# Performance work log

Measured on AMD Instinct MI355X. Metric: run time of the kernel, lower is better.

## Reference

```python
import jax, jax.numpy as jnp
import numpy as np

K_ORDER = 3
GRID_N = 10
GRID_LO, GRID_HI = -2.0, 2.0
LAYERS = [(49, 256), (256, 256), (256, 10)]
NCOEF = GRID_N + K_ORDER  # 13


def mish(x):
    return x * jnp.tanh(jax.nn.softplus(x))


def bspline_basis(x):
    # x: (B, in) -> basis (B, in, GRID_N + K_ORDER)
    h = (GRID_HI - GRID_LO) / GRID_N
    knots = GRID_LO + h * jnp.arange(-K_ORDER, GRID_N + K_ORDER + 1, dtype=x.dtype)  # (G+2k+1,)
    xx = x[..., None]
    B = ((xx >= knots[:-1]) & (xx < knots[1:])).astype(x.dtype)  # degree-0, (B,in,G+2k)
    for d in range(1, K_ORDER + 1):
        left = (xx - knots[: -(d + 1)]) / (knots[d:-1] - knots[: -(d + 1)]) * B[..., :-1]
        right = (knots[d + 1:] - xx) / (knots[d + 1:] - knots[1:-d]) * B[..., 1:]
        B = left + right
    return B  # (B, in, G+k)


def kan_layer(x, coef, scale_base, scale_sp, bias):
    # x: (B,in); coef: (in,out,G+k); scales: (in,out); bias: (out,)
    basis = bspline_basis(x)                                   # (B,in,G+k)
    spline = jnp.einsum('big,iog->bo', basis, coef * scale_sp[..., None])
    base = jnp.einsum('bi,io->bo', mish(x), scale_base)
    return base + spline + bias


def setup_inputs() -> dict:
    key = jax.random.key(0)
    ks = jax.random.split(key, 1 + 4 * len(LAYERS))
    inp = {'x': jax.random.normal(ks[0], (8192, 1, 28, 28), dtype=jnp.float32)}
    i = 1
    for li, (fin, fout) in enumerate(LAYERS, start=1):
        inp[f'coef{li}'] = 0.1 * jax.random.normal(ks[i], (fin, fout, NCOEF), dtype=jnp.float32); i += 1
        inp[f'sb{li}'] = 1.0 + 0.1 * jax.random.normal(ks[i], (fin, fout), dtype=jnp.float32); i += 1
        inp[f'sp{li}'] = 1.0 + 0.1 * jax.random.normal(ks[i], (fin, fout), dtype=jnp.float32); i += 1
        inp[f'b{li}'] = jnp.zeros((fout,), dtype=jnp.float32); i += 1
    return inp


def reference(x, coef1, sb1, sp1, b1, coef2, sb2, sp2, b2, coef3, sb3, sp3, b3):
    B = x.shape[0]
    # avg_pool2d(x, 4): 28x28 -> 7x7
    h = x.reshape(B, 1, 7, 4, 7, 4).mean(axis=(3, 5))
    h = h.reshape(B, 49)
    h = kan_layer(h, coef1, sb1, sp1, b1)
    h = kan_layer(h, coef2, sb2, sp2, b2)
    h = kan_layer(h, coef3, sb3, sp3, b3)
    return jax.nn.log_softmax(h, axis=1)
```

## Files before the change

### kernel.cpp

```cpp
#include <hip/hip_runtime.h>
#include <hip/hip_bf16.h>

typedef __bf16 bf16x8_t __attribute__((ext_vector_type(8)));
typedef float f32x4_t __attribute__((ext_vector_type(4)));
using bf16 = __hip_bfloat16;

__device__ __forceinline__ unsigned short f2bf_bits(float v) {
  __hip_bfloat16 h = __float2bfloat16(v);
  return *reinterpret_cast<unsigned short*>(&h);
}

__device__ __forceinline__ float mish_f(float x) {
  float z = __expf(x);
  float n = z * (z + 2.0f);
  float m = x * n / (n + 2.0f);
  return (x > 10.0f) ? x : m;
}

__device__ __forceinline__ void kan_feats28(bf16* dst, float x) {
  unsigned int* d32 = (unsigned int*)dst;
#pragma unroll
  for (int d = 0; d < 7; ++d) d32[d] = 0u;
  float t = (x + 3.2f) * 2.5f;
  if (t >= 0.0f && t < 16.0f) {
    float tf = floorf(t);
    int c = (int)tf;
    float u = t - tf;
    float um = 1.0f - u;
    float u2 = u * u, u3 = u2 * u;
    const float s6 = 1.0f / 6.0f;
    float w0 = um * um * um * s6;
    float w1 = (3.0f * u3 - 6.0f * u2 + 4.0f) * s6;
    float w2 = (-3.0f * u3 + 3.0f * u2 + 3.0f * u + 1.0f) * s6;
    float w3 = u3 * s6;
    int j0 = c - 3;
    if (j0 >= 0)               dst[j0]     = __float2bfloat16(w0);
    if (j0 >= -1 && j0 <= 11)  dst[j0 + 1] = __float2bfloat16(w1);
    if (j0 >= -2 && j0 <= 10)  dst[j0 + 2] = __float2bfloat16(w2);
    if (j0 <= 9)               dst[j0 + 3] = __float2bfloat16(w3);
  }
  dst[13] = __float2bfloat16(mish_f(x));
}

__global__ __launch_bounds__(256) void prep_all(
    const float* __restrict__ c1, const float* __restrict__ sb1, const float* __restrict__ sp1,
    const float* __restrict__ c2, const float* __restrict__ sb2, const float* __restrict__ sp2,
    const float* __restrict__ c3, const float* __restrict__ sb3, const float* __restrict__ sp3,
    bf16* __restrict__ W1f, bf16* __restrict__ W2f, bf16* __restrict__ W3f) {
  const int b = blockIdx.x, t = threadIdx.x;
  float vals[14];
  if (b < 49) {
    const int i = b, o = t;
    const int ntg = o >> 4, lrr = o & 15;
    const size_t io = (size_t)i * 256 + o;
    const float spv = sp1[io];
#pragma unroll
    for (int r = 0; r < 13; ++r) vals[r] = c1[io * 13 + r] * spv;
    vals[13] = sb1[io];
#pragma unroll
    for (int d = 0; d < 7; ++d) {
      const int k2 = i * 14 + 2 * d;
      const int s = k2 >> 5, r2 = k2 & 31;
      const size_t off = ((size_t)(s * 16 + ntg)) * 512 + lrr * 32 + (r2 >> 3) * 8 + (r2 & 7);
      *(unsigned int*)(W1f + off) = (unsigned int)f2bf_bits(vals[2 * d]) |
                                    ((unsigned int)f2bf_bits(vals[2 * d + 1]) << 16);
    }
  } else if (b == 49) {
    const int ntg = t >> 4, lrr = t & 15;
#pragma unroll
    for (int d = 0; d < 9; ++d) {
      const int k2 = 686 + 2 * d;
      const int r2 = k2 & 31;
      *(unsigned int*)(W1f + ((size_t)(21 * 16 + ntg)) * 512 + lrr * 32 + (r2 >> 3) * 8 + (r2 & 7)) = 0u;
    }
  } else if (b < 562) {
    if (t >= 128) return;
    const int idx = b - 50;
    const int i = idx >> 1;
    const int o = (idx & 1) * 128 + t;
    const int ntg = o >> 4, lrr = o & 15;
    const size_t io = (size_t)i * 256 + o;
    const float spv = sp2[io];
#pragma unroll
    for (int r = 0; r < 13; ++r) vals[r] = c2[io * 13 + r] * spv;
    vals[13] = sb2[io];
#pragma unroll
    for (int d = 0; d < 7; ++d) {
      const int k2 = i * 14 + 2 * d;
      const int s = k2 >> 5, r2 = k2 & 31;
      const size_t off = ((size_t)(s * 16 + ntg)) * 512 + lrr * 32 + (r2 >> 3) * 8 + (r2 & 7);
      *(unsigned int*)(W2f + off) = (unsigned int)f2bf_bits(vals[2 * d]) |
                                    ((unsigned int)f2bf_bits(vals[2 * d + 1]) << 16);
    }
  } else {
    const int i = b - 562, o = t;
    if (o < 10) {
      const size_t io = (size_t)i * 10 + o;
      const float spv = sp3[io];
#pragma unroll
      for (int r = 0; r < 13; ++r) vals[r] = c3[io * 13 + r] * spv;
      vals[13] = sb3[io];
#pragma unroll
      for (int d = 0; d < 7; ++d) {
        const int k2 = i * 14 + 2 * d;
        const int s = k2 >> 5, r2 = k2 & 31;
        const size_t off = (size_t)s * 512 + o * 32 + (r2 >> 3) * 8 + (r2 & 7);
        *(unsigned int*)(W3f + off) = (unsigned int)f2bf_bits(vals[2 * d]) |
                                      ((unsigned int)f2bf_bits(vals[2 * d + 1]) << 16);
      }
    } else if (o < 16) {
#pragma unroll
      for (int d = 0; d < 7; ++d) {
        const int k2 = i * 14 + 2 * d;
        const int s = k2 >> 5, r2 = k2 & 31;
        *(unsigned int*)(W3f + (size_t)s * 512 + o * 32 + (r2 >> 3) * 8 + (r2 & 7)) = 0u;
      }
    }
  }
}

__global__ __launch_bounds__(1024, 4) void meganet(
    const float* __restrict__ x, const bf16* __restrict__ W1f,
    const bf16* __restrict__ W2f, const bf16* __restrict__ W3f,
    const float* __restrict__ b1, const float* __restrict__ b2,
    const float* __restrict__ b3, float* __restrict__ out) {
  __shared__ __align__(16) char lds[73728];
  float* const Hs = (float*)lds;
  bf16* const Ach0 = (bf16*)(lds + 36864);
  bf16* const Ach1 = (bf16*)(lds + 51712);
  float* const P = (float*)(lds + 66560);
  float* const xs = (float*)lds;
  float* const Red = (float*)(lds + 36864);
  float* const V = (float*)(lds + 51712);

  const int t = threadIdx.x;
  const int w = t >> 6, lane = t & 63, quad = lane >> 4, lr = lane & 15;
  const int tr = (t >> 4) & 31, ej = t & 15;
  const int r0 = blockIdx.x * 32;
  const int foff = lr * 32 + quad * 8;
  const bool cons = (w < 8);
  const int ntg0 = 2 * w;

  for (int h = 0; h < 2; ++h) {
    const float4* src = (const float4*)x + (size_t)(r0 + h * 16) * 196;
    float4* xd = (float4*)xs;
#pragma unroll
    for (int l = 0; l < 4; ++l) {
      const int idx = t + l * 1024;
      if (idx < 3136) xd[idx] = src[idx];
    }
    __syncthreads();
    if (t < 784) {
      const int img = t / 49, p = t - img * 49;
      const int oh = p / 7, ow = p - oh * 7;
      const float* xi = xs + img * 784 + oh * 112 + ow * 4;
      float s = 0.f;
#pragma unroll
      for (int rr = 0; rr < 4; ++rr)
#pragma unroll
        for (int cc = 0; cc < 4; ++cc) s += xi[rr * 28 + cc];
      P[(h * 16 + img) * 56 + p] = s * (1.0f / 16.0f);
    }
    __syncthreads();
  }

  f32x4_t acc[2][2];
#pragma unroll
  for (int m = 0; m < 2; ++m)
#pragma unroll
    for (int n = 0; n < 2; ++n) acc[m][n] = (f32x4_t){0.f, 0.f, 0.f, 0.f};

  bf16x8_t q0[4], q1[4];
  if (cons) {
#pragma unroll
    for (int s = 0; s < 4; ++s) {
      q0[s] = *(const bf16x8_t*)(W1f + (size_t)(s * 16 + ntg0) * 512 + foff);
      q1[s] = *(const bf16x8_t*)(W1f + (size_t)(s * 16 + ntg0 + 1) * 512 + foff);
    }
  } else {
    kan_feats28(Ach0 + tr * 232 + ej * 14, P[tr * 56 + ej]);
  }
  __syncthreads();
#pragma unroll
  for (int c = 0; c < 4; ++c) {
    const bf16* const Ac = (c & 1) ? Ach1 : Ach0;
    bf16* const An = (c & 1) ? Ach0 : Ach1;
    if (cons) {
      const int nks = (c < 3) ? 7 : 1;
#pragma unroll
      for (int ks = 0; ks < 7; ++ks) {
        if (ks >= nks) continue;
        const int kk = c * 7 + ks;
        const int sl = kk & 3;
        bf16x8_t bb0 = q0[sl], bb1 = q1[sl];
        if (kk + 4 < 22) {
          q0[sl] = *(const bf16x8_t*)(W1f + (size_t)((kk + 4) * 16 + ntg0) * 512 + foff);
          q1[sl] = *(const bf16x8_t*)(W1f + (size_t)((kk + 4) * 16 + ntg0 + 1) * 512 + foff);
        }
#pragma unroll
        for (int m = 0; m < 2; ++m) {
          bf16x8_t a = *(const bf16x8_t*)(Ac + (m * 16 + lr) * 232 + ks * 32 + quad * 8);
          acc[m][0] = __builtin_amdgcn_mfma_f32_16x16x32_bf16(a, bb0, acc[m][0], 0, 0, 0);
          acc[m][1] = __builtin_amdgcn_mfma_f32_16x16x32_bf16(a, bb1, acc[m][1], 0, 0, 0);
        }
      }
    } else {
      if (c < 2) {
        kan_feats28(An + tr * 232 + ej * 14, P[tr * 56 + (c + 1) * 16 + ej]);
      } else if (c == 2) {
        if (ej == 0) kan_feats28(An + tr * 232, P[tr * 56 + 48]);
        else if (ej == 1) {
          unsigned int* z = (unsigned int*)(An + tr * 232 + 14);
#pragma unroll
          for (int d = 0; d < 9; ++d) z[d] = 0u;
        }
      }
    }
    __syncthreads();
  }
  if (cons) {
#pragma unroll
    for (int m = 0; m < 2; ++m)
#pragma unroll
      for (int n = 0; n < 2; ++n) {
        const int col = w * 32 + n * 16 + lr;
        const float bn = b1[col];
        f32x4_t v;
#pragma unroll
        for (int r = 0; r < 4; ++r) v[r] = acc[m][n][r] + bn;
        *(f32x4_t*)(Hs + col * 36 + m * 16 + quad * 4) = v;
      }
  }
  __syncthreads();

#pragma unroll
  for (int m = 0; m < 2; ++m)
#pragma unroll
    for (int n = 0; n < 2; ++n) acc[m][n] = (f32x4_t){0.f, 0.f, 0.f, 0.f};
  if (cons) {
#pragma unroll
    for (int s = 0; s < 4; ++s) {
      q0[s] = *(const bf16x8_t*)(W2f + (size_t)(s * 16 + ntg0) * 512 + foff);
      q1[s] = *(const bf16x8_t*)(W2f + (size_t)(s * 16 + ntg0 + 1) * 512 + foff);
    }
  } else {
    kan_feats28(Ach0 + tr * 232 + ej * 14, Hs[ej * 36 + tr]);
  }
  __syncthreads();
#pragma unroll
  for (int c = 0; c < 16; ++c) {
    const bf16* const Ac = (c & 1) ? Ach1 : Ach0;
    bf16* const An = (c & 1) ? Ach0 : Ach1;
    if (cons) {
#pragma unroll
      for (int ks = 0; ks < 7; ++ks) {
        const int kk = c * 7 + ks;
        const int sl = kk & 3;
        bf16x8_t bb0 = q0[sl], bb1 = q1[sl];
        if (kk + 4 < 112) {
          q0[sl] = *(const bf16x8_t*)(W2f + (size_t)((kk + 4) * 16 + ntg0) * 512 + foff);
          q1[sl] = *(const bf16x8_t*)(W2f + (size_t)((kk + 4) * 16 + ntg0 + 1) * 512 + foff);
        }
#pragma unroll
        for (int m = 0; m < 2; ++m) {
          bf16x8_t a = *(const bf16x8_t*)(Ac + (m * 16 + lr) * 232 + ks * 32 + quad * 8);
          acc[m][0] = __builtin_amdgcn_mfma_f32_16x16x32_bf16(a, bb0, acc[m][0], 0, 0, 0);
          acc[m][1] = __builtin_amdgcn_mfma_f32_16x16x32_bf16(a, bb1, acc[m][1], 0, 0, 0);
        }
      }
    } else if (c < 15) {
      kan_feats28(An + tr * 232 + ej * 14, Hs[((c + 1) * 16 + ej) * 36 + tr]);
    }
    __syncthreads();
  }
  if (cons) {
#pragma unroll
    for (int m = 0; m < 2; ++m)
#pragma unroll
      for (int n = 0; n < 2; ++n) {
        const int col = w * 32 + n * 16 + lr;
        const float bn = b2[col];
        f32x4_t v;
#pragma unroll
        for (int r = 0; r < 4; ++r) v[r] = acc[m][n][r] + bn;
        *(f32x4_t*)(Hs + col * 36 + m * 16 + quad * 4) = v;
      }
  }
  __syncthreads();

  f32x4_t acc3[2];
  acc3[0] = (f32x4_t){0.f, 0.f, 0.f, 0.f};
  acc3[1] = acc3[0];
  bf16x8_t q3[4];
  if (w < 7) {
#pragma unroll
    for (int s = 0; s < 4; ++s)
      q3[s] = *(const bf16x8_t*)(W3f + (size_t)(s * 7 + w) * 512 + foff);
  } else if (!cons) {
    kan_feats28(Ach0 + tr * 232 + ej * 14, Hs[ej * 36 + tr]);
  }
  __syncthreads();
#pragma unroll
  for (int c = 0; c < 16; ++c) {
    const bf16* const Ac = (c & 1) ? Ach1 : Ach0;
    bf16* const An = (c & 1) ? Ach0 : Ach1;
    if (w < 7) {
      bf16x8_t bb = q3[c & 3];
      if (c + 4 < 16)
        q3[c & 3] = *(const bf16x8_t*)(W3f + (size_t)((c + 4) * 7 + w) * 512 + foff);
#pragma unroll
      for (int m = 0; m < 2; ++m) {
        bf16x8_t a = *(const bf16x8_t*)(Ac + (m * 16 + lr) * 232 + w * 32 + quad * 8);
        acc3[m] = __builtin_amdgcn_mfma_f32_16x16x32_bf16(a, bb, acc3[m], 0, 0, 0);
      }
    } else if (!cons && c < 15) {
      kan_feats28(An + tr * 232 + ej * 14, Hs[((c + 1) * 16 + ej) * 36 + tr]);
    }
    __syncthreads();
  }
  if (w < 7) {
#pragma unroll
    for (int m = 0; m < 2; ++m)
#pragma unroll
      for (int r = 0; r < 4; ++r)
        Red[w * 512 + (m * 16 + quad * 4 + r) * 16 + lr] = acc3[m][r];
  }
  __syncthreads();
  if (t < 512) {
    float s = (ej < 10) ? b3[ej] : 0.f;
#pragma unroll
    for (int ks = 0; ks < 7; ++ks) s += Red[ks * 512 + tr * 16 + ej];
    V[tr * 16 + ej] = s;
  }
  __syncthreads();
  if (t < 32) {
    float vv[10];
#pragma unroll
    for (int o = 0; o < 10; ++o) vv[o] = V[t * 16 + o];
    float mx = vv[0];
#pragma unroll
    for (int o = 1; o < 10; ++o) mx = fmaxf(mx, vv[o]);
    float se = 0.f;
#pragma unroll
    for (int o = 0; o < 10; ++o) se += expf(vv[o] - mx);
    const float l = mx + logf(se);
#pragma unroll
    for (int o = 0; o < 10; ++o) out[(size_t)(r0 + t) * 10 + o] = vv[o] - l;
  }
}

extern "C" void kernel_launch(void* const* d_in, const int* in_sizes, int n_in,
                              void* d_out, int out_size, void* d_ws, size_t ws_size,
                              hipStream_t stream) {
  const float* x = (const float*)d_in[0];
  const float* coef1 = (const float*)d_in[1];
  const float* sb1 = (const float*)d_in[2];
  const float* sp1 = (const float*)d_in[3];
  const float* b1 = (const float*)d_in[4];
  const float* coef2 = (const float*)d_in[5];
  const float* sb2 = (const float*)d_in[6];
  const float* sp2 = (const float*)d_in[7];
  const float* b2 = (const float*)d_in[8];
  const float* coef3 = (const float*)d_in[9];
  const float* sb3 = (const float*)d_in[10];
  const float* sp3 = (const float*)d_in[11];
  const float* b3 = (const float*)d_in[12];
  float* out = (float*)d_out;

  char* ws = (char*)d_ws;
  bf16* W1f = (bf16*)ws;
  bf16* W2f = (bf16*)(ws + 360448);
  bf16* W3f = (bf16*)(ws + 2195456);

  prep_all<<<818, 256, 0, stream>>>(coef1, sb1, sp1, coef2, sb2, sp2,
                                    coef3, sb3, sp3, W1f, W2f, W3f);
  meganet<<<256, 1024, 0, stream>>>(x, W1f, W2f, W3f, b1, b2, b3, out);
}
```

Baseline: 139.0 us.

## Double chunk size in layers 2-3, halve barriers, use lightweight LDS-only barrier

Layers 2 and 3 now process 32 input features per chunk instead of 16, so the producer waves build two feature rows each step and the number of block barriers in those loops is halved. The LDS A-tile stride grows to 474 and shared memory grows to about 102 KB to hold the larger double buffers. The weight prefetch depth in layer 2 rises from 4 to 6 slots. __syncthreads is replaced by a custom barrier that waits only on lgkmcnt, not on outstanding global loads. The larger LDS footprint may reduce blocks per CU, and the custom barrier depends on no global-memory ordering being needed across it.

```diff
diff --git a/kernel.cpp b/kernel.cpp
--- a/kernel.cpp
+++ b/kernel.cpp
@@ -4,6 +4,10 @@
 typedef __bf16 bf16x8_t __attribute__((ext_vector_type(8)));
 typedef float f32x4_t __attribute__((ext_vector_type(4)));
 using bf16 = __hip_bfloat16;
+
+__device__ __forceinline__ void softbar() {
+  asm volatile("s_waitcnt lgkmcnt(0)\n\ts_barrier" ::: "memory");
+}
 
 __device__ __forceinline__ unsigned short f2bf_bits(float v) {
   __hip_bfloat16 h = __float2bfloat16(v);
@@ -124,14 +128,14 @@
     const bf16* __restrict__ W2f, const bf16* __restrict__ W3f,
     const float* __restrict__ b1, const float* __restrict__ b2,
     const float* __restrict__ b3, float* __restrict__ out) {
-  __shared__ __align__(16) char lds[73728];
+  __shared__ __align__(16) char lds[104704];
   float* const Hs = (float*)lds;
   bf16* const Ach0 = (bf16*)(lds + 36864);
-  bf16* const Ach1 = (bf16*)(lds + 51712);
-  float* const P = (float*)(lds + 66560);
+  bf16* const Ach1 = (bf16*)(lds + 67200);
+  float* const P = (float*)(lds + 97536);
   float* const xs = (float*)lds;
   float* const Red = (float*)(lds + 36864);
-  float* const V = (float*)(lds + 51712);
+  float* const V = (float*)(lds + 51200);
 
   const int t = threadIdx.x;
   const int w = t >> 6, lane = t & 63, quad = lane >> 4, lr = lane & 15;
@@ -149,7 +153,7 @@
       const int idx = t + l * 1024;
       if (idx < 3136) xd[idx] = src[idx];
     }
-    __syncthreads();
+    softbar();
     if (t < 784) {
       const int img = t / 49, p = t - img * 49;
       const int oh = p / 7, ow = p - oh * 7;
@@ -161,7 +165,7 @@
         for (int cc = 0; cc < 4; ++cc) s += xi[rr * 28 + cc];
       P[(h * 16 + img) * 56 + p] = s * (1.0f / 16.0f);
     }
-    __syncthreads();
+    softbar();
   }
 
   f32x4_t acc[2][2];
@@ -170,7 +174,8 @@
 #pragma unroll
     for (int n = 0; n < 2; ++n) acc[m][n] = (f32x4_t){0.f, 0.f, 0.f, 0.f};
 
-  bf16x8_t q0[4], q1[4];
+  bf16x8_t q0[6], q1[6];
+
   if (cons) {
 #pragma unroll
     for (int s = 0; s < 4; ++s) {
@@ -178,9 +183,9 @@
       q1[s] = *(const bf16x8_t*)(W1f + (size_t)(s * 16 + ntg0 + 1) * 512 + foff);
     }
   } else {
-    kan_feats28(Ach0 + tr * 232 + ej * 14, P[tr * 56 + ej]);
-  }
-  __syncthreads();
+    kan_feats28(Ach0 + tr * 474 + ej * 14, P[tr * 56 + ej]);
+  }
+  softbar();
 #pragma unroll
   for (int c = 0; c < 4; ++c) {
     const bf16* const Ac = (c & 1) ? Ach1 : Ach0;
@@ -199,24 +204,24 @@
         }
 #pragma unroll
         for (int m = 0; m < 2; ++m) {
-          bf16x8_t a = *(const bf16x8_t*)(Ac + (m * 16 + lr) * 232 + ks * 32 + quad * 8);
+          bf16x8_t a = *(const bf16x8_t*)(Ac + (m * 16 + lr) * 474 + ks * 32 + quad * 8);
           acc[m][0] = __builtin_amdgcn_mfma_f32_16x16x32_bf16(a, bb0, acc[m][0], 0, 0, 0);
           acc[m][1] = __builtin_amdgcn_mfma_f32_16x16x32_bf16(a, bb1, acc[m][1], 0, 0, 0);
         }
       }
     } else {
       if (c < 2) {
-        kan_feats28(An + tr * 232 + ej * 14, P[tr * 56 + (c + 1) * 16 + ej]);
+        kan_feats28(An + tr * 474 + ej * 14, P[tr * 56 + (c + 1) * 16 + ej]);
       } else if (c == 2) {
-        if (ej == 0) kan_feats28(An + tr * 232, P[tr * 56 + 48]);
+        if (ej == 0) kan_feats28(An + tr * 474, P[tr * 56 + 48]);
         else if (ej == 1) {
-          unsigned int* z = (unsigned int*)(An + tr * 232 + 14);
+          unsigned int* z = (unsigned int*)(An + tr * 474 + 14);
 #pragma unroll
           for (int d = 0; d < 9; ++d) z[d] = 0u;
         }
       }
     }
-    __syncthreads();
+    softbar();
   }
   if (cons) {
 #pragma unroll
@@ -231,7 +236,7 @@
         *(f32x4_t*)(Hs + col * 36 + m * 16 + quad * 4) = v;
       }
   }
-  __syncthreads();
+  softbar();
 
 #pragma unroll
   for (int m = 0; m < 2; ++m)
@@ -239,39 +244,42 @@
     for (int n = 0; n < 2; ++n) acc[m][n] = (f32x4_t){0.f, 0.f, 0.f, 0.f};
   if (cons) {
 #pragma unroll
-    for (int s = 0; s < 4; ++s) {
+    for (int s = 0; s < 6; ++s) {
       q0[s] = *(const bf16x8_t*)(W2f + (size_t)(s * 16 + ntg0) * 512 + foff);
       q1[s] = *(const bf16x8_t*)(W2f + (size_t)(s * 16 + ntg0 + 1) * 512 + foff);
     }
   } else {
-    kan_feats28(Ach0 + tr * 232 + ej * 14, Hs[ej * 36 + tr]);
-  }
-  __syncthreads();
-#pragma unroll
-  for (int c = 0; c < 16; ++c) {
+    kan_feats28(Ach0 + tr * 474 + ej * 14, Hs[ej * 36 + tr]);
+    kan_feats28(Ach0 + tr * 474 + (ej + 16) * 14, Hs[(ej + 16) * 36 + tr]);
+  }
+  softbar();
+#pragma unroll
+  for (int c = 0; c < 8; ++c) {
     const bf16* const Ac = (c & 1) ? Ach1 : Ach0;
     bf16* const An = (c & 1) ? Ach0 : Ach1;
     if (cons) {
 #pragma unroll
-      for (int ks = 0; ks < 7; ++ks) {
-        const int kk = c * 7 + ks;
-        const int sl = kk & 3;
+      for (int j = 0; j < 14; ++j) {
+        const int kk = c * 14 + j;
+        const int sl = kk % 6;
         bf16x8_t bb0 = q0[sl], bb1 = q1[sl];
-        if (kk + 4 < 112) {
-          q0[sl] = *(const bf16x8_t*)(W2f + (size_t)((kk + 4) * 16 + ntg0) * 512 + foff);
-          q1[sl] = *(const bf16x8_t*)(W2f + (size_t)((kk + 4) * 16 + ntg0 + 1) * 512 + foff);
+        if (kk + 6 < 112) {
+          q0[sl] = *(const bf16x8_t*)(W2f + (size_t)((kk + 6) * 16 + ntg0) * 512 + foff);
+          q1[sl] = *(const bf16x8_t*)(W2f + (size_t)((kk + 6) * 16 + ntg0 + 1) * 512 + foff);
         }
 #pragma unroll
         for (int m = 0; m < 2; ++m) {
-          bf16x8_t a = *(const bf16x8_t*)(Ac + (m * 16 + lr) * 232 + ks * 32 + quad * 8);
+          bf16x8_t a = *(const bf16x8_t*)(Ac + (m * 16 + lr) * 474 + j * 32 + quad * 8);
           acc[m][0] = __builtin_amdgcn_mfma_f32_16x16x32_bf16(a, bb0, acc[m][0], 0, 0, 0);
           acc[m][1] = __builtin_amdgcn_mfma_f32_16x16x32_bf16(a, bb1, acc[m][1], 0, 0, 0);
         }
       }
-    } else if (c < 15) {
-      kan_feats28(An + tr * 232 + ej * 14, Hs[((c + 1) * 16 + ej) * 36 + tr]);
-    }
-    __syncthreads();
+    } else if (c < 7) {
+      const int i0 = (c + 1) * 32 + ej;
+      kan_feats28(An + tr * 474 + ej * 14, Hs[i0 * 36 + tr]);
+      kan_feats28(An + tr * 474 + (ej + 16) * 14, Hs[(i0 + 16) * 36 + tr]);
+    }
+    softbar();
   }
   if (cons) {
 #pragma unroll
@@ -286,7 +294,7 @@
         *(f32x4_t*)(Hs + col * 36 + m * 16 + quad * 4) = v;
       }
   }
-  __syncthreads();
+  softbar();
 
   f32x4_t acc3[2];
   acc3[0] = (f32x4_t){0.f, 0.f, 0.f, 0.f};
@@ -294,29 +302,39 @@
   bf16x8_t q3[4];
   if (w < 7) {
 #pragma unroll
-    for (int s = 0; s < 4; ++s)
-      q3[s] = *(const bf16x8_t*)(W3f + (size_t)(s * 7 + w) * 512 + foff);
+    for (int cc = 0; cc < 2; ++cc) {
+      q3[cc * 2] = *(const bf16x8_t*)(W3f + (size_t)(cc * 14 + w) * 512 + foff);
+      q3[cc * 2 + 1] = *(const bf16x8_t*)(W3f + (size_t)(cc * 14 + 7 + w) * 512 + foff);
+    }
   } else if (!cons) {
-    kan_feats28(Ach0 + tr * 232 + ej * 14, Hs[ej * 36 + tr]);
-  }
-  __syncthreads();
-#pragma unroll
-  for (int c = 0; c < 16; ++c) {
+    kan_feats28(Ach0 + tr * 474 + ej * 14, Hs[ej * 36 + tr]);
+    kan_feats28(Ach0 + tr * 474 + (ej + 16) * 14, Hs[(ej + 16) * 36 + tr]);
+  }
+  softbar();
+#pragma unroll
+  for (int c = 0; c < 8; ++c) {
     const bf16* const Ac = (c & 1) ? Ach1 : Ach0;
     bf16* const An = (c & 1) ? Ach0 : Ach1;
     if (w < 7) {
-      bf16x8_t bb = q3[c & 3];
-      if (c + 4 < 16)
-        q3[c & 3] = *(const bf16x8_t*)(W3f + (size_t)((c + 4) * 7 + w) * 512 + foff);
+      const int p = (c & 1) * 2;
+      bf16x8_t bb0 = q3[p], bb1 = q3[p + 1];
+      if (c + 2 < 8) {
+        q3[p] = *(const bf16x8_t*)(W3f + (size_t)((c + 2) * 14 + w) * 512 + foff);
+        q3[p + 1] = *(const bf16x8_t*)(W3f + (size_t)((c + 2) * 14 + 7 + w) * 512 + foff);
+      }
 #pragma unroll
       for (int m = 0; m < 2; ++m) {
-        bf16x8_t a = *(const bf16x8_t*)(Ac + (m * 16 + lr) * 232 + w * 32 + quad * 8);
-        acc3[m] = __builtin_amdgcn_mfma_f32_16x16x32_bf16(a, bb, acc3[m], 0, 0, 0);
-      }
-    } else if (!cons && c < 15) {
-      kan_feats28(An + tr * 232 + ej * 14, Hs[((c + 1) * 16 + ej) * 36 + tr]);
-    }
-    __syncthreads();
+        bf16x8_t a0 = *(const bf16x8_t*)(Ac + (m * 16 + lr) * 474 + w * 32 + quad * 8);
+        bf16x8_t a1 = *(const bf16x8_t*)(Ac + (m * 16 + lr) * 474 + (7 + w) * 32 + quad * 8);
+        acc3[m] = __builtin_amdgcn_mfma_f32_16x16x32_bf16(a0, bb0, acc3[m], 0, 0, 0);
+        acc3[m] = __builtin_amdgcn_mfma_f32_16x16x32_bf16(a1, bb1, acc3[m], 0, 0, 0);
+      }
+    } else if (!cons && c < 7) {
+      const int i0 = (c + 1) * 32 + ej;
+      kan_feats28(An + tr * 474 + ej * 14, Hs[i0 * 36 + tr]);
+      kan_feats28(An + tr * 474 + (ej + 16) * 14, Hs[(i0 + 16) * 36 + tr]);
+    }
+    softbar();
   }
   if (w < 7) {
 #pragma unroll
@@ -325,14 +343,14 @@
       for (int r = 0; r < 4; ++r)
         Red[w * 512 + (m * 16 + quad * 4 + r) * 16 + lr] = acc3[m][r];
   }
-  __syncthreads();
+  softbar();
   if (t < 512) {
     float s = (ej < 10) ? b3[ej] : 0.f;
 #pragma unroll
     for (int ks = 0; ks < 7; ++ks) s += Red[ks * 512 + tr * 16 + ej];
     V[tr * 16 + ej] = s;
   }
-  __syncthreads();
+  softbar();
   if (t < 32) {
     float vv[10];
 #pragma unroll
```

Measured after the change: 185.2 us. +33.3%, slower.

## Halve rows per block and merge producer/consumer warps in fused KAN kernel

Applied to the files above, without the earlier changes.

The fused KAN kernel now handles 16 rows per block with 512 threads instead of 32 rows with 1024 threads, and launches 512 blocks instead of 256. The separate producer warps that built B-spline features are removed. All 8 warps now run the MFMAs, and the first 256 threads also compute the next chunk's features after their MFMAs. This halves LDS use and doubles the grid to spread work over more CUs. In exchange, each weight fetch from global memory/L2 is reused over half as many rows, and feature building is no longer overlapped by dedicated warps.

```diff
diff --git a/kernel.cpp b/kernel.cpp
--- a/kernel.cpp
+++ b/kernel.cpp
@@ -119,38 +119,37 @@
   }
 }
 
-__global__ __launch_bounds__(1024, 4) void meganet(
+__global__ __launch_bounds__(512, 4) void meganet(
     const float* __restrict__ x, const bf16* __restrict__ W1f,
     const bf16* __restrict__ W2f, const bf16* __restrict__ W3f,
     const float* __restrict__ b1, const float* __restrict__ b2,
     const float* __restrict__ b3, float* __restrict__ out) {
-  __shared__ __align__(16) char lds[73728];
+  __shared__ __align__(16) char lds[38912];
   float* const Hs = (float*)lds;
-  bf16* const Ach0 = (bf16*)(lds + 36864);
-  bf16* const Ach1 = (bf16*)(lds + 51712);
-  float* const P = (float*)(lds + 66560);
+  bf16* const Ach0 = (bf16*)(lds + 20480);
+  bf16* const Ach1 = (bf16*)(lds + 27904);
+  float* const P = (float*)(lds + 35328);
   float* const xs = (float*)lds;
-  float* const Red = (float*)(lds + 36864);
-  float* const V = (float*)(lds + 51712);
+  float* const Red = (float*)(lds + 20480);
+  float* const V = (float*)(lds + 27904);
 
   const int t = threadIdx.x;
   const int w = t >> 6, lane = t & 63, quad = lane >> 4, lr = lane & 15;
-  const int tr = (t >> 4) & 31, ej = t & 15;
-  const int r0 = blockIdx.x * 32;
+  const int tr = (t >> 4) & 15, ej = t & 15;
+  const int r0 = blockIdx.x * 16;
   const int foff = lr * 32 + quad * 8;
-  const bool cons = (w < 8);
   const int ntg0 = 2 * w;
 
   for (int h = 0; h < 2; ++h) {
-    const float4* src = (const float4*)x + (size_t)(r0 + h * 16) * 196;
+    const float4* src = (const float4*)x + (size_t)(r0 + h * 8) * 196;
     float4* xd = (float4*)xs;
 #pragma unroll
     for (int l = 0; l < 4; ++l) {
-      const int idx = t + l * 1024;
-      if (idx < 3136) xd[idx] = src[idx];
-    }
-    __syncthreads();
-    if (t < 784) {
+      const int idx = t + l * 512;
+      if (idx < 1568) xd[idx] = src[idx];
+    }
+    __syncthreads();
+    if (t < 392) {
       const int img = t / 49, p = t - img * 49;
       const int oh = p / 7, ow = p - oh * 7;
       const float* xi = xs + img * 784 + oh * 112 + ow * 4;
@@ -159,52 +158,43 @@
       for (int rr = 0; rr < 4; ++rr)
 #pragma unroll
         for (int cc = 0; cc < 4; ++cc) s += xi[rr * 28 + cc];
-      P[(h * 16 + img) * 56 + p] = s * (1.0f / 16.0f);
-    }
-    __syncthreads();
-  }
-
-  f32x4_t acc[2][2];
-#pragma unroll
-  for (int m = 0; m < 2; ++m)
-#pragma unroll
-    for (int n = 0; n < 2; ++n) acc[m][n] = (f32x4_t){0.f, 0.f, 0.f, 0.f};
-
+      P[(h * 8 + img) * 56 + p] = s * (1.0f / 16.0f);
+    }
+    __syncthreads();
+  }
+
+  f32x4_t acc[2];
+  acc[0] = (f32x4_t){0.f, 0.f, 0.f, 0.f};
+  acc[1] = acc[0];
   bf16x8_t q0[4], q1[4];
-  if (cons) {
-#pragma unroll
-    for (int s = 0; s < 4; ++s) {
-      q0[s] = *(const bf16x8_t*)(W1f + (size_t)(s * 16 + ntg0) * 512 + foff);
-      q1[s] = *(const bf16x8_t*)(W1f + (size_t)(s * 16 + ntg0 + 1) * 512 + foff);
-    }
-  } else {
-    kan_feats28(Ach0 + tr * 232 + ej * 14, P[tr * 56 + ej]);
-  }
+
+#pragma unroll
+  for (int s = 0; s < 4; ++s) {
+    q0[s] = *(const bf16x8_t*)(W1f + (size_t)(s * 16 + ntg0) * 512 + foff);
+    q1[s] = *(const bf16x8_t*)(W1f + (size_t)(s * 16 + ntg0 + 1) * 512 + foff);
+  }
+  if (t < 256) kan_feats28(Ach0 + tr * 232 + ej * 14, P[tr * 56 + ej]);
   __syncthreads();
 #pragma unroll
   for (int c = 0; c < 4; ++c) {
     const bf16* const Ac = (c & 1) ? Ach1 : Ach0;
     bf16* const An = (c & 1) ? Ach0 : Ach1;
-    if (cons) {
-      const int nks = (c < 3) ? 7 : 1;
-#pragma unroll
-      for (int ks = 0; ks < 7; ++ks) {
-        if (ks >= nks) continue;
-        const int kk = c * 7 + ks;
-        const int sl = kk & 3;
-        bf16x8_t bb0 = q0[sl], bb1 = q1[sl];
-        if (kk + 4 < 22) {
-          q0[sl] = *(const bf16x8_t*)(W1f + (size_t)((kk + 4) * 16 + ntg0) * 512 + foff);
-          q1[sl] = *(const bf16x8_t*)(W1f + (size_t)((kk + 4) * 16 + ntg0 + 1) * 512 + foff);
-        }
-#pragma unroll
-        for (int m = 0; m < 2; ++m) {
-          bf16x8_t a = *(const bf16x8_t*)(Ac + (m * 16 + lr) * 232 + ks * 32 + quad * 8);
-          acc[m][0] = __builtin_amdgcn_mfma_f32_16x16x32_bf16(a, bb0, acc[m][0], 0, 0, 0);
-          acc[m][1] = __builtin_amdgcn_mfma_f32_16x16x32_bf16(a, bb1, acc[m][1], 0, 0, 0);
-        }
-      }
-    } else {
+    const int nks = (c < 3) ? 7 : 1;
+#pragma unroll
+    for (int ks = 0; ks < 7; ++ks) {
+      if (ks >= nks) continue;
+      const int kk = c * 7 + ks;
+      const int sl = kk & 3;
+      bf16x8_t bb0 = q0[sl], bb1 = q1[sl];
+      if (kk + 4 < 22) {
+        q0[sl] = *(const bf16x8_t*)(W1f + (size_t)((kk + 4) * 16 + ntg0) * 512 + foff);
+        q1[sl] = *(const bf16x8_t*)(W1f + (size_t)((kk + 4) * 16 + ntg0 + 1) * 512 + foff);
+      }
+      bf16x8_t a = *(const bf16x8_t*)(Ac + lr * 232 + ks * 32 + quad * 8);
+      acc[0] = __builtin_amdgcn_mfma_f32_16x16x32_bf16(a, bb0, acc[0], 0, 0, 0);
+      acc[1] = __builtin_amdgcn_mfma_f32_16x16x32_bf16(a, bb1, acc[1], 0, 0, 0);
+    }
+    if (t < 256) {
       if (c < 2) {
         kan_feats28(An + tr * 232 + ej * 14, P[tr * 56 + (c + 1) * 16 + ej]);
       } else if (c == 2) {
@@ -218,87 +208,66 @@
     }
     __syncthreads();
   }
-  if (cons) {
-#pragma unroll
-    for (int m = 0; m < 2; ++m)
-#pragma unroll
-      for (int n = 0; n < 2; ++n) {
-        const int col = w * 32 + n * 16 + lr;
-        const float bn = b1[col];
-        f32x4_t v;
-#pragma unroll
-        for (int r = 0; r < 4; ++r) v[r] = acc[m][n][r] + bn;
-        *(f32x4_t*)(Hs + col * 36 + m * 16 + quad * 4) = v;
-      }
-  }
-  __syncthreads();
-
-#pragma unroll
-  for (int m = 0; m < 2; ++m)
-#pragma unroll
-    for (int n = 0; n < 2; ++n) acc[m][n] = (f32x4_t){0.f, 0.f, 0.f, 0.f};
-  if (cons) {
-#pragma unroll
-    for (int s = 0; s < 4; ++s) {
-      q0[s] = *(const bf16x8_t*)(W2f + (size_t)(s * 16 + ntg0) * 512 + foff);
-      q1[s] = *(const bf16x8_t*)(W2f + (size_t)(s * 16 + ntg0 + 1) * 512 + foff);
-    }
-  } else {
-    kan_feats28(Ach0 + tr * 232 + ej * 14, Hs[ej * 36 + tr]);
-  }
+#pragma unroll
+  for (int n = 0; n < 2; ++n) {
+    const int col = w * 32 + n * 16 + lr;
+    const float bn = b1[col];
+    f32x4_t v;
+#pragma unroll
+    for (int r = 0; r < 4; ++r) v[r] = acc[n][r] + bn;
+    *(f32x4_t*)(Hs + col * 20 + quad * 4) = v;
+  }
+  __syncthreads();
+
+  acc[0] = (f32x4_t){0.f, 0.f, 0.f, 0.f};
+  acc[1] = acc[0];
+#pragma unroll
+  for (int s = 0; s < 4; ++s) {
+    q0[s] = *(const bf16x8_t*)(W2f + (size_t)(s * 16 + ntg0) * 512 + foff);
+    q1[s] = *(const bf16x8_t*)(W2f + (size_t)(s * 16 + ntg0 + 1) * 512 + foff);
+  }
+  if (t < 256) kan_feats28(Ach0 + tr * 232 + ej * 14, Hs[ej * 20 + tr]);
   __syncthreads();
 #pragma unroll
   for (int c = 0; c < 16; ++c) {
     const bf16* const Ac = (c & 1) ? Ach1 : Ach0;
     bf16* const An = (c & 1) ? Ach0 : Ach1;
-    if (cons) {
-#pragma unroll
-      for (int ks = 0; ks < 7; ++ks) {
-        const int kk = c * 7 + ks;
-        const int sl = kk & 3;
-        bf16x8_t bb0 = q0[sl], bb1 = q1[sl];
-        if (kk + 4 < 112) {
-          q0[sl] = *(const bf16x8_t*)(W2f + (size_t)((kk + 4) * 16 + ntg0) * 512 + foff);
-          q1[sl] = *(const bf16x8_t*)(W2f + (size_t)((kk + 4) * 16 + ntg0 + 1) * 512 + foff);
-        }
-#pragma unroll
-        for (int m = 0; m < 2; ++m) {
-          bf16x8_t a = *(const bf16x8_t*)(Ac + (m * 16 + lr) * 232 + ks * 32 + quad * 8);
-          acc[m][0] = __builtin_amdgcn_mfma_f32_16x16x32_bf16(a, bb0, acc[m][0], 0, 0, 0);
-          acc[m][1] = __builtin_amdgcn_mfma_f32_16x16x32_bf16(a, bb1, acc[m][1], 0, 0, 0);
-        }
-      }
-    } else if (c < 15) {
-      kan_feats28(An + tr * 232 + ej * 14, Hs[((c + 1) * 16 + ej) * 36 + tr]);
-    }
-    __syncthreads();
-  }
-  if (cons) {
-#pragma unroll
-    for (int m = 0; m < 2; ++m)
-#pragma unroll
-      for (int n = 0; n < 2; ++n) {
-        const int col = w * 32 + n * 16 + lr;
-        const float bn = b2[col];
-        f32x4_t v;
-#pragma unroll
-        for (int r = 0; r < 4; ++r) v[r] = acc[m][n][r] + bn;
-        *(f32x4_t*)(Hs + col * 36 + m * 16 + quad * 4) = v;
-      }
-  }
-  __syncthreads();
-
-  f32x4_t acc3[2];
-  acc3[0] = (f32x4_t){0.f, 0.f, 0.f, 0.f};
-  acc3[1] = acc3[0];
+#pragma unroll
+    for (int ks = 0; ks < 7; ++ks) {
+      const int kk = c * 7 + ks;
+      const int sl = kk & 3;
+      bf16x8_t bb0 = q0[sl], bb1 = q1[sl];
+      if (kk + 4 < 112) {
+        q0[sl] = *(const bf16x8_t*)(W2f + (size_t)((kk + 4) * 16 + ntg0) * 512 + foff);
+        q1[sl] = *(const bf16x8_t*)(W2f + (size_t)((kk + 4) * 16 + ntg0 + 1) * 512 + foff);
+      }
+      bf16x8_t a = *(const bf16x8_t*)(Ac + lr * 232 + ks * 32 + quad * 8);
+      acc[0] = __builtin_amdgcn_mfma_f32_16x16x32_bf16(a, bb0, acc[0], 0, 0, 0);
+      acc[1] = __builtin_amdgcn_mfma_f32_16x16x32_bf16(a, bb1, acc[1], 0, 0, 0);
+    }
+    if (t < 256 && c < 15)
+      kan_feats28(An + tr * 232 + ej * 14, Hs[((c + 1) * 16 + ej) * 20 + tr]);
+    __syncthreads();
+  }
+#pragma unroll
+  for (int n = 0; n < 2; ++n) {
+    const int col = w * 32 + n * 16 + lr;
+    const float bn = b2[col];
+    f32x4_t v;
+#pragma unroll
+    for (int r = 0; r < 4; ++r) v[r] = acc[n][r] + bn;
+    *(f32x4_t*)(Hs + col * 20 + quad * 4) = v;
+  }
+  __syncthreads();
+
+  f32x4_t acc3 = {0.f, 0.f, 0.f, 0.f};
   bf16x8_t q3[4];
   if (w < 7) {
 #pragma unroll
     for (int s = 0; s < 4; ++s)
       q3[s] = *(const bf16x8_t*)(W3f + (size_t)(s * 7 + w) * 512 + foff);
-  } else if (!cons) {
-    kan_feats28(Ach0 + tr * 232 + ej * 14, Hs[ej * 36 + tr]);
-  }
+  }
+  if (t < 256) kan_feats28(Ach0 + tr * 232 + ej * 14, Hs[ej * 20 + tr]);
   __syncthreads();
 #pragma unroll
   for (int c = 0; c < 16; ++c) {
@@ -308,32 +277,27 @@
       bf16x8_t bb = q3[c & 3];
       if (c + 4 < 16)
         q3[c & 3] = *(const bf16x8_t*)(W3f + (size_t)((c + 4) * 7 + w) * 512 + foff);
-#pragma unroll
-      for (int m = 0; m < 2; ++m) {
-        bf16x8_t a = *(const bf16x8_t*)(Ac + (m * 16 + lr) * 232 + w * 32 + quad * 8);
-        acc3[m] = __builtin_amdgcn_mfma_f32_16x16x32_bf16(a, bb, acc3[m], 0, 0, 0);
-      }
-    } else if (!cons && c < 15) {
-      kan_feats28(An + tr * 232 + ej * 14, Hs[((c + 1) * 16 + ej) * 36 + tr]);
-    }
+      bf16x8_t a = *(const bf16x8_t*)(Ac + lr * 232 + w * 32 + quad * 8);
+      acc3 = __builtin_amdgcn_mfma_f32_16x16x32_bf16(a, bb, acc3, 0, 0, 0);
+    }
+    if (t < 256 && c < 15)
+      kan_feats28(An + tr * 232 + ej * 14, Hs[((c + 1) * 16 + ej) * 20 + tr]);
     __syncthreads();
   }
   if (w < 7) {
 #pragma unroll
-    for (int m = 0; m < 2; ++m)
-#pragma unroll
-      for (int r = 0; r < 4; ++r)
-        Red[w * 512 + (m * 16 + quad * 4 + r) * 16 + lr] = acc3[m][r];
-  }
-  __syncthreads();
-  if (t < 512) {
+    for (int r = 0; r < 4; ++r)
+      Red[w * 256 + (quad * 4 + r) * 16 + lr] = acc3[r];
+  }
+  __syncthreads();
+  if (t < 256) {
     float s = (ej < 10) ? b3[ej] : 0.f;
 #pragma unroll
-    for (int ks = 0; ks < 7; ++ks) s += Red[ks * 512 + tr * 16 + ej];
+    for (int ks = 0; ks < 7; ++ks) s += Red[ks * 256 + tr * 16 + ej];
     V[tr * 16 + ej] = s;
   }
   __syncthreads();
-  if (t < 32) {
+  if (t < 16) {
     float vv[10];
 #pragma unroll
     for (int o = 0; o < 10; ++o) vv[o] = V[t * 16 + o];
@@ -374,5 +338,5 @@
 
   prep_all<<<818, 256, 0, stream>>>(coef1, sb1, sp1, coef2, sb2, sp2,
                                     coef3, sb3, sp3, W1f, W2f, W3f);
-  meganet<<<256, 1024, 0, stream>>>(x, W1f, W2f, W3f, b1, b2, b3, out);
-}
+  meganet<<<512, 512, 0, stream>>>(x, W1f, W2f, W3f, b1, b2, b3, out);
+}
```

Measured after the change: 164.8 us. 1.19x slower.
